# Kernel optimization log

Measured on AMD Instinct MI355X. Metric: run time of the kernel, lower is better.

Reference implementation:

```python
import jax, jax.numpy as jnp
import numpy as np

B, T, E = 2, 2048, 1024
H, D = 16, 64
NH = H * D  # num_hiddens
EPS = 1e-5


def setup_inputs() -> dict:
    key = jax.random.key(0)
    ks = jax.random.split(key, 8)
    s = 1.0 / np.sqrt(E)
    inputs_q = jax.random.normal(ks[0], (B, T, E), dtype=jnp.float32)
    inputs_kv = jax.random.normal(ks[1], (B, T, E), dtype=jnp.float32)
    # torch Linear weights: [out_features, in_features]
    wq = jax.random.uniform(ks[2], (NH, E), jnp.float32, -s, s)
    wk = jax.random.uniform(ks[3], (NH, E), jnp.float32, -s, s)
    wv = jax.random.uniform(ks[4], (NH, E), jnp.float32, -s, s)
    wo = jax.random.uniform(ks[5], (E, NH), jnp.float32, -1.0 / np.sqrt(NH), 1.0 / np.sqrt(NH))
    q_ln_scale = jnp.ones((NH,), jnp.float32)
    q_ln_bias = jnp.zeros((NH,), jnp.float32)
    k_ln_scale = jnp.ones((NH,), jnp.float32)
    k_ln_bias = jnp.zeros((NH,), jnp.float32)
    # causal mask, broadcastable over heads: [B, 1, T, T]
    mask = jnp.broadcast_to(jnp.tril(jnp.ones((T, T), dtype=bool)), (B, 1, T, T))
    return dict(inputs_q=inputs_q, inputs_kv=inputs_kv, mask=mask,
                wq=wq, wk=wk, wv=wv, wo=wo,
                q_ln_scale=q_ln_scale, q_ln_bias=q_ln_bias,
                k_ln_scale=k_ln_scale, k_ln_bias=k_ln_bias)


def _layernorm(x, scale, bias):
    mu = jnp.mean(x, axis=-1, keepdims=True)
    var = jnp.var(x, axis=-1, keepdims=True)
    return (x - mu) * jax.lax.rsqrt(var + EPS) * scale + bias


def reference(inputs_q, inputs_kv, mask, wq, wk, wv, wo,
              q_ln_scale, q_ln_bias, k_ln_scale, k_ln_bias):
    q = jnp.einsum('bte,he->bth', inputs_q, wq)   # [B,T,NH]
    k = jnp.einsum('bte,he->bth', inputs_kv, wk)
    q = _layernorm(q, q_ln_scale, q_ln_bias)
    k = _layernorm(k, k_ln_scale, k_ln_bias)
    v = jnp.einsum('bte,he->bth', inputs_kv, wv)
    q = q.reshape(B, T, H, D)
    k = k.reshape(B, T, H, D)
    v = v.reshape(B, T, H, D)
    attn = jnp.einsum('bthd,bThd->bhtT', q, k) * (1.0 / np.sqrt(D))
    attn = jnp.where(mask, attn, -jnp.inf)
    p = jax.nn.softmax(attn, axis=-1)
    out = jnp.einsum('bhtT,bThd->bthd', p, v).reshape(B, T, NH)
    return jnp.einsum('bth,eh->bte', out, wo)
```

## Files before the change

kernel.cpp:

```cpp
#include <hip/hip_runtime.h>
#include <stdint.h>

#define BB 2
#define TT 2048
#define EE 1024
#define HH 16
#define DD 64
#define NHH 1024
#define BT 4096
#define NT 32

typedef unsigned short u16_t;
typedef __bf16 bf16_t;
typedef bf16_t bf16x8 __attribute__((ext_vector_type(8)));
typedef bf16_t bf16x4 __attribute__((ext_vector_type(4)));
typedef float f32x4 __attribute__((ext_vector_type(4)));

__device__ __forceinline__ u16_t f2bf(float f) {
  union { float f; uint32_t u; } v; v.f = f;
  return (u16_t)((v.u + 0x7fffu + ((v.u >> 16) & 1u)) >> 16);
}

__device__ __forceinline__ uint32_t cvtpk_bf16(float lo, float hi) {
  uint32_t r;
  asm("v_cvt_pk_bf16_f32 %0, %1, %2" : "=v"(r) : "v"(lo), "v"(hi));
  return r;
}

__device__ __forceinline__ void gl_lds16(const u16_t* g, u16_t* l) {
  __builtin_amdgcn_global_load_lds(
      (const __attribute__((address_space(1))) uint32_t*)g,
      (__attribute__((address_space(3))) uint32_t*)l, 16, 0, 0);
}

__global__ __launch_bounds__(256) void cvt_all(const float* __restrict__ inq,
                                               const float* __restrict__ inkv,
                                               const float* __restrict__ wq,
                                               const float* __restrict__ wk,
                                               const float* __restrict__ wv,
                                               const float* __restrict__ wo,
                                               u16_t* __restrict__ Xq,
                                               u16_t* __restrict__ Xkv,
                                               u16_t* __restrict__ Wqkv,
                                               u16_t* __restrict__ Wo) {
  const int NX = BT * NHH / 4;
  const int NW = NHH * EE / 4;
  const int total = 2 * NX + 4 * NW;
  for (int idx = blockIdx.x * 256 + threadIdx.x; idx < total; idx += gridDim.x * 256) {
    const float* src; u16_t* dst; int off;
    if (idx < NX)            { src = inq;  dst = Xq;  off = idx; }
    else if (idx < 2 * NX)   { src = inkv; dst = Xkv; off = idx - NX; }
    else if (idx < 2 * NX + NW)     { src = wq; dst = Wqkv;                       off = idx - 2 * NX; }
    else if (idx < 2 * NX + 2 * NW) { src = wk; dst = Wqkv + (size_t)NHH * EE;    off = idx - (2 * NX + NW); }
    else if (idx < 2 * NX + 3 * NW) { src = wv; dst = Wqkv + (size_t)2 * NHH * EE; off = idx - (2 * NX + 2 * NW); }
    else                            { src = wo; dst = Wo;                          off = idx - (2 * NX + 3 * NW); }
    float4 v = ((const float4*)src)[off];
    ushort4 o;
    o.x = f2bf(v.x); o.y = f2bf(v.y); o.z = f2bf(v.z); o.w = f2bf(v.w);
    ((ushort4*)dst)[off] = o;
  }
}

__global__ __launch_bounds__(256, 3) void gemm_qkv(const u16_t* __restrict__ Xq,
                                                   const u16_t* __restrict__ Xkv,
                                                   const u16_t* __restrict__ Wqkv,
                                                   u16_t* __restrict__ Qpre,
                                                   u16_t* __restrict__ Kpre,
                                                   u16_t* __restrict__ Vt) {
  __shared__ __align__(16) u16_t As[128 * 64];
  __shared__ __align__(16) u16_t Bs[128 * 64];
  const int tid = threadIdx.x;
  const int lane = tid & 63;
  const int w = tid >> 6;
  const int wm = w >> 1, wn = w & 1;
  const int nt = blockIdx.x, mt = blockIdx.y;
  const int l15 = lane & 15, l4 = lane >> 4;
  const int band = nt >> 3;
  const u16_t* A = (band == 0) ? Xq : Xkv;
  const int ncol0 = (nt & 7) * 128;

  f32x4 acc[4][4] = {};
  for (int ks = 0; ks < 16; ++ks) {
    const int k0 = ks << 6;
#pragma unroll
    for (int i = 0; i < 4; ++i) {
      int ci = i * 256 + w * 64 + lane;
      int row = ci >> 3, c8 = ci & 7;
      int c8s = c8 ^ (row & 7);
      gl_lds16(A + (size_t)(mt * 128 + row) * EE + k0 + c8s * 8,
               &As[(i * 256 + w * 64) * 8]);
      gl_lds16(Wqkv + (size_t)(nt * 128 + row) * EE + k0 + c8s * 8,
               &Bs[(i * 256 + w * 64) * 8]);
    }
    __syncthreads();
#pragma unroll
    for (int kt = 0; kt < 2; ++kt) {
      bf16x8 af[4], bfr[4];
#pragma unroll
      for (int m = 0; m < 4; ++m) {
        int r = wm * 64 + m * 16 + l15;
        af[m] = *(const bf16x8*)&As[r * 64 + ((kt * 4 + l4) ^ (r & 7)) * 8];
      }
#pragma unroll
      for (int n = 0; n < 4; ++n) {
        int r = wn * 64 + n * 16 + l15;
        bfr[n] = *(const bf16x8*)&Bs[r * 64 + ((kt * 4 + l4) ^ (r & 7)) * 8];
      }
#pragma unroll
      for (int m = 0; m < 4; ++m)
#pragma unroll
        for (int n = 0; n < 4; ++n)
          acc[m][n] = __builtin_amdgcn_mfma_f32_16x16x32_bf16(af[m], bfr[n], acc[m][n], 0, 0, 0);
    }
    __syncthreads();
  }
  if (band < 2) {
    u16_t* C = (band == 0) ? Qpre : Kpre;
#pragma unroll
    for (int m = 0; m < 4; ++m)
#pragma unroll
      for (int n = 0; n < 4; ++n)
#pragma unroll
        for (int r = 0; r < 4; ++r) {
          int row = mt * 128 + wm * 64 + m * 16 + l4 * 4 + r;
          int col = ncol0 + wn * 64 + n * 16 + l15;
          C[(size_t)row * NHH + col] = f2bf(acc[m][n][r]);
        }
  } else {
#pragma unroll
    for (int m = 0; m < 4; ++m)
#pragma unroll
      for (int n = 0; n < 4; ++n) {
        int rt = mt * 128 + wm * 64 + m * 16 + l4 * 4;
        int col = ncol0 + wn * 64 + n * 16 + l15;
        int bq = rt >> 11, t0 = rt & (TT - 1);
        int hh = col >> 6, dd = col & 63;
        ushort4 o;
        o.x = f2bf(acc[m][n][0]);
        o.y = f2bf(acc[m][n][1]);
        o.z = f2bf(acc[m][n][2]);
        o.w = f2bf(acc[m][n][3]);
        *(ushort4*)&Vt[((size_t)(bq * HH + hh) * 64 + dd) * TT + t0] = o;
      }
  }
}

__global__ __launch_bounds__(256, 3) void gemm_out(const u16_t* __restrict__ A,
                                                   const u16_t* __restrict__ W,
                                                   float* __restrict__ C) {
  __shared__ __align__(16) u16_t As[64 * 64];
  __shared__ __align__(16) u16_t Bs[128 * 64];
  const int tid = threadIdx.x;
  const int lane = tid & 63;
  const int w = tid >> 6;
  const int wm = w >> 1, wn = w & 1;
  const int nt = blockIdx.x, mt = blockIdx.y;
  const int l15 = lane & 15, l4 = lane >> 4;

  f32x4 acc[2][4] = {};
  for (int ks = 0; ks < 16; ++ks) {
    const int k0 = ks << 6;
#pragma unroll
    for (int i = 0; i < 6; ++i) {
      int ci = i * 256 + w * 64 + lane;
      if (i < 2) {
        int row = ci >> 3, c8s = (ci & 7) ^ ((ci >> 3) & 7);
        gl_lds16(A + (size_t)(mt * 64 + row) * NHH + k0 + c8s * 8,
                 &As[(i * 256 + w * 64) * 8]);
      } else {
        int cj = ci - 512;
        int row = cj >> 3, c8s = (cj & 7) ^ ((cj >> 3) & 7);
        gl_lds16(W + (size_t)(nt * 128 + row) * NHH + k0 + c8s * 8,
                 &Bs[(i * 256 + w * 64 - 512) * 8]);
      }
    }
    __syncthreads();
#pragma unroll
    for (int kt = 0; kt < 2; ++kt) {
      bf16x8 af[2], bfr[4];
#pragma unroll
      for (int m = 0; m < 2; ++m) {
        int r = wm * 32 + m * 16 + l15;
        af[m] = *(const bf16x8*)&As[r * 64 + ((kt * 4 + l4) ^ (r & 7)) * 8];
      }
#pragma unroll
      for (int n = 0; n < 4; ++n) {
        int r = wn * 64 + n * 16 + l15;
        bfr[n] = *(const bf16x8*)&Bs[r * 64 + ((kt * 4 + l4) ^ (r & 7)) * 8];
      }
#pragma unroll
      for (int m = 0; m < 2; ++m)
#pragma unroll
        for (int n = 0; n < 4; ++n)
          acc[m][n] = __builtin_amdgcn_mfma_f32_16x16x32_bf16(af[m], bfr[n], acc[m][n], 0, 0, 0);
    }
    __syncthreads();
  }
#pragma unroll
  for (int m = 0; m < 2; ++m)
#pragma unroll
    for (int n = 0; n < 4; ++n)
#pragma unroll
      for (int r = 0; r < 4; ++r) {
        int row = mt * 64 + wm * 32 + m * 16 + l4 * 4 + r;
        int col = nt * 128 + wn * 64 + n * 16 + l15;
        C[(size_t)row * NHH + col] = acc[m][n][r];
      }
}

__global__ __launch_bounds__(256) void ln_both(const u16_t* __restrict__ Qpre,
                                               const u16_t* __restrict__ Kpre,
                                               const float* __restrict__ qs,
                                               const float* __restrict__ qb,
                                               const float* __restrict__ ks,
                                               const float* __restrict__ kb,
                                               u16_t* __restrict__ Qln,
                                               u16_t* __restrict__ Kln) {
  int which = blockIdx.y;
  const u16_t* X = which ? Kpre : Qpre;
  const float* scale = which ? ks : qs;
  const float* bias = which ? kb : qb;
  u16_t* Y = which ? Kln : Qln;
  int row = blockIdx.x;
  int tid = threadIdx.x;
  ushort4 v4 = ((const ushort4*)(X + (size_t)row * NHH))[tid];
  float x[4];
  {
    union { uint32_t u; float f; } c;
    c.u = (uint32_t)v4.x << 16; x[0] = c.f;
    c.u = (uint32_t)v4.y << 16; x[1] = c.f;
    c.u = (uint32_t)v4.z << 16; x[2] = c.f;
    c.u = (uint32_t)v4.w << 16; x[3] = c.f;
  }
  float s = x[0] + x[1] + x[2] + x[3];
  float sq = x[0] * x[0] + x[1] * x[1] + x[2] * x[2] + x[3] * x[3];
#pragma unroll
  for (int m = 1; m < 64; m <<= 1) {
    s += __shfl_xor(s, m);
    sq += __shfl_xor(sq, m);
  }
  __shared__ float ss[4], ssq[4];
  int w = tid >> 6;
  if ((tid & 63) == 0) { ss[w] = s; ssq[w] = sq; }
  __syncthreads();
  s = ss[0] + ss[1] + ss[2] + ss[3];
  sq = ssq[0] + ssq[1] + ssq[2] + ssq[3];
  float mean = s * (1.0f / 1024.0f);
  float var = sq * (1.0f / 1024.0f) - mean * mean;
  float rstd = rsqrtf(var + 1e-5f);
  float4 sc = ((const float4*)scale)[tid];
  float4 bi = ((const float4*)bias)[tid];
  ushort4 o;
  o.x = f2bf((x[0] - mean) * rstd * sc.x + bi.x);
  o.y = f2bf((x[1] - mean) * rstd * sc.y + bi.y);
  o.z = f2bf((x[2] - mean) * rstd * sc.z + bi.z);
  o.w = f2bf((x[3] - mean) * rstd * sc.w + bi.w);
  ((ushort4*)Y)[(size_t)row * 256 + tid] = o;
}

__global__ __launch_bounds__(512, 6) void attn_fwd(const u16_t* __restrict__ Q,
                                                   const u16_t* __restrict__ K,
                                                   const u16_t* __restrict__ Vt,
                                                   u16_t* __restrict__ O) {
  __shared__ __align__(16) u16_t Ks[2][64 * 64];
  __shared__ __align__(16) u16_t Vs[2][64 * 64];
  const int bh = blockIdx.x;
  const int qt = NT - 1 - (int)blockIdx.y;
  const int b = bh >> 4, h = bh & 15;
  const int tid = threadIdx.x, lane = tid & 63, w = tid >> 6;
  const int l15 = lane & 15, l4 = lane >> 4;
  const int qsub = w & 3, par = w >> 2;
  const float SCALE = 0.125f * 1.44269504f;

  const int q0 = qt * 64 + qsub * 16;
  const int myq = q0 + l15;

  bf16x8 qf[2];
#pragma unroll
  for (int kt = 0; kt < 2; ++kt) {
    bf16x8 t = *(const bf16x8*)&Q[(size_t)(b * TT + myq) * NHH + h * 64 + kt * 32 + l4 * 8];
    union { bf16x8 v; uint32_t u[4]; } tt;
    tt.v = t;
#pragma unroll
    for (int d2 = 0; d2 < 4; ++d2) {
      union { uint32_t u; float f; } lo, hi;
      lo.u = tt.u[d2] << 16;
      hi.u = tt.u[d2] & 0xffff0000u;
      tt.u[d2] = cvtpk_bf16(lo.f * SCALE, hi.f * SCALE);
    }
    qf[kt] = tt.v;
  }

  const int ci = tid;
  const int rowk = ci >> 3;
  const int c8k = (ci & 7) ^ (rowk & 7);
  const int c8v = (ci & 7) ^ ((rowk >> 1) & 7);
  const u16_t* kp = K + (size_t)(b * TT + rowk) * NHH + h * 64 + c8k * 8;
  const u16_t* vp = Vt + ((size_t)bh * 64 + rowk) * TT + c8v * 8;
  u16_t* kdst0 = &Ks[0][ci * 8];
  u16_t* kdst1 = &Ks[1][ci * 8];
  u16_t* vdst0 = &Vs[0][ci * 8];
  u16_t* vdst1 = &Vs[1][ci * 8];
  const u16_t* myK = Ks[par];
  const u16_t* myV = Vs[par];

  f32x4 accO[4] = {};
  float lrow = 0.f;

  const int ntile = qt + 1;
  const int nph = (ntile + 1) >> 1;

  for (int ph = 0; ph < nph; ++ph) {
    const int t1ok = (2 * ph + 1) < ntile;
    gl_lds16(kp, kdst0);
    gl_lds16(vp, vdst0);
    if (t1ok) {
      gl_lds16(kp + 64 * NHH, kdst1);
      gl_lds16(vp + 64, vdst1);
    }
    kp += 128 * NHH;
    vp += 128;
    __syncthreads();

    const int t = 2 * ph + par;
    if (t < ntile) {
      const int kb = t * 64;
      const bool masked = (t == qt);
      const int nact = masked ? (qsub + 1) : 4;
      const int ktlim = masked ? ((qsub >> 1) + 1) : 2;

      f32x4 s[4];
      __builtin_amdgcn_s_setprio(1);
#pragma unroll
      for (int n = 0; n < 4; ++n) {
        if (n < nact) {
          s[n] = (f32x4){0.f, 0.f, 0.f, 0.f};
#pragma unroll
          for (int kt = 0; kt < 2; ++kt) {
            int r = n * 16 + l15;
            bf16x8 kf = *(const bf16x8*)&myK[r * 64 + ((kt * 4 + l4) ^ (r & 7)) * 8];
            s[n] = __builtin_amdgcn_mfma_f32_16x16x32_bf16(kf, qf[kt], s[n], 0, 0, 0);
          }
        }
      }
      __builtin_amdgcn_s_setprio(0);
      if (masked) {
#pragma unroll
        for (int n = 0; n < 4; ++n)
          if (n < nact)
#pragma unroll
            for (int r = 0; r < 4; ++r)
              if (kb + n * 16 + l4 * 4 + r > myq) s[n][r] = -3e38f;
      }
      float tsum = 0.f;
#pragma unroll
      for (int n = 0; n < 4; ++n)
        if (n < nact)
#pragma unroll
          for (int r = 0; r < 4; ++r) {
            float p = exp2f(s[n][r]);
            s[n][r] = p;
            tsum += p;
          }
      tsum += __shfl_xor(tsum, 16);
      tsum += __shfl_xor(tsum, 32);
      lrow += tsum;
#pragma unroll
      for (int n = 0; n < 4; ++n)
        if (n >= nact && n < 2 * ktlim) s[n] = (f32x4){0.f, 0.f, 0.f, 0.f};

      __builtin_amdgcn_s_setprio(1);
#pragma unroll
      for (int kt = 0; kt < 2; ++kt) {
        if (kt < ktlim) {
          union { uint32_t u[4]; bf16x8 v; } pa;
          pa.u[0] = cvtpk_bf16(s[2 * kt][0], s[2 * kt][1]);
          pa.u[1] = cvtpk_bf16(s[2 * kt][2], s[2 * kt][3]);
          pa.u[2] = cvtpk_bf16(s[2 * kt + 1][0], s[2 * kt + 1][1]);
          pa.u[3] = cvtpk_bf16(s[2 * kt + 1][2], s[2 * kt + 1][3]);
#pragma unroll
          for (int dn = 0; dn < 4; ++dn) {
            int drow = dn * 16 + l15;
            int vm = l15 & 14;
            int pg0 = (kt * 8 + l4) ^ vm;
            int pg1 = (kt * 8 + 4 + l4) ^ vm;
            union { bf16x4 hh[2]; bf16x8 v; } vf;
            vf.hh[0] = *(const bf16x4*)&myV[drow * 64 + pg0 * 4];
            vf.hh[1] = *(const bf16x4*)&myV[drow * 64 + pg1 * 4];
            accO[dn] = __builtin_amdgcn_mfma_f32_16x16x32_bf16(pa.v, vf.v, accO[dn], 0, 0, 0);
          }
        }
      }
      __builtin_amdgcn_s_setprio(0);
    }
    __syncthreads();
  }

  float* xch = (float*)&Ks[0][0];
  if (par == 1) {
    float* dst = xch + (qsub * 64 + lane) * 20;
#pragma unroll
    for (int dn = 0; dn < 4; ++dn) *(f32x4*)(dst + dn * 4) = accO[dn];
    if (l4 == 0) xch[5120 + qsub * 16 + l15] = lrow;
  } else {
    if (l4 == 0) xch[5184 + qsub * 16 + l15] = lrow;
  }
  __syncthreads();
  if (par == 0) {
    const float* src = xch + (qsub * 64 + lane) * 20;
    f32x4 acc1[4];
#pragma unroll
    for (int dn = 0; dn < 4; ++dn) acc1[dn] = *(const f32x4*)(src + dn * 4);
#pragma unroll
    for (int r = 0; r < 4; ++r) {
      int q = l4 * 4 + r;
      float l0 = xch[5184 + qsub * 16 + q];
      float l1 = xch[5120 + qsub * 16 + q];
      float rinv = 1.0f / (l0 + l1);
      int row = b * TT + q0 + q;
#pragma unroll
      for (int dn = 0; dn < 4; ++dn) {
        float o = (accO[dn][r] + acc1[dn][r]) * rinv;
        O[(size_t)row * NHH + h * 64 + dn * 16 + l15] = f2bf(o);
      }
    }
  }
}

extern "C" void kernel_launch(void* const* d_in, const int* in_sizes, int n_in,
                              void* d_out, int out_size, void* d_ws, size_t ws_size,
                              hipStream_t stream) {
  const float* inq = (const float*)d_in[0];
  const float* inkv = (const float*)d_in[1];
  const float* wq = (const float*)d_in[3];
  const float* wk = (const float*)d_in[4];
  const float* wv = (const float*)d_in[5];
  const float* wo = (const float*)d_in[6];
  const float* qs = (const float*)d_in[7];
  const float* qb = (const float*)d_in[8];
  const float* kls = (const float*)d_in[9];
  const float* klb = (const float*)d_in[10];
  float* out = (float*)d_out;

  uint8_t* ws = (uint8_t*)d_ws;
  const size_t SZ_X = (size_t)BT * NHH * 2;
  const size_t SZ_W = (size_t)NHH * EE * 2;
  u16_t* Xq   = (u16_t*)(ws);
  u16_t* Xkv  = (u16_t*)(ws + SZ_X);
  u16_t* Wqkv = (u16_t*)(ws + 2 * SZ_X);
  u16_t* Wo   = (u16_t*)(ws + 2 * SZ_X + 3 * SZ_W);
  u16_t* Qpre = (u16_t*)(ws + 2 * SZ_X + 4 * SZ_W);
  u16_t* Kpre = (u16_t*)(ws + 3 * SZ_X + 4 * SZ_W);
  u16_t* Qln  = (u16_t*)(ws + 4 * SZ_X + 4 * SZ_W);
  u16_t* Kln  = (u16_t*)(ws + 5 * SZ_X + 4 * SZ_W);
  u16_t* Vt   = (u16_t*)(ws + 6 * SZ_X + 4 * SZ_W);
  u16_t* AOut = (u16_t*)(ws + 7 * SZ_X + 4 * SZ_W);

  cvt_all<<<3072, 256, 0, stream>>>(inq, inkv, wq, wk, wv, wo, Xq, Xkv, Wqkv, Wo);

  gemm_qkv<<<dim3(24, 32), 256, 0, stream>>>(Xq, Xkv, Wqkv, Qpre, Kpre, Vt);

  ln_both<<<dim3(BT, 2), 256, 0, stream>>>(Qpre, Kpre, qs, qb, kls, klb, Qln, Kln);

  attn_fwd<<<dim3(BB * HH, NT), 512, 0, stream>>>(Qln, Kln, Vt, AOut);

  gemm_out<<<dim3(8, 64), 256, 0, stream>>>(AOut, Wo, out);
}
```

Before: 231.6 us.

## Widen attention KV tiles to 128 per wave group and coalesce V-transpose stores

The attention kernel now loads 256 keys per phase (two 128-key halves, one per wave parity) instead of 128. This halves the number of barrier/load phases and doubles the MFMA work per sync. Causal masking now uses a per-subtile relative offset. Occupancy is lowered from 6 to 4 blocks per CU because of the larger LDS footprint. Separately, the QKV GEMM's V output is transposed through shared memory so each thread writes contiguous 16-byte chunks, replacing scattered 8-byte stores.

```diff
diff --git a/kernel.cpp b/kernel.cpp
--- a/kernel.cpp
+++ b/kernel.cpp
@@ -67,8 +67,9 @@
                                                    u16_t* __restrict__ Qpre,
                                                    u16_t* __restrict__ Kpre,
                                                    u16_t* __restrict__ Vt) {
-  __shared__ __align__(16) u16_t As[128 * 64];
-  __shared__ __align__(16) u16_t Bs[128 * 64];
+  __shared__ __align__(16) u16_t smem[128 * 136];
+  u16_t* As = smem;
+  u16_t* Bs = smem + 8192;
   const int tid = threadIdx.x;
   const int lane = tid & 63;
   const int w = tid >> 6;
@@ -131,17 +132,23 @@
     for (int m = 0; m < 4; ++m)
 #pragma unroll
       for (int n = 0; n < 4; ++n) {
-        int rt = mt * 128 + wm * 64 + m * 16 + l4 * 4;
-        int col = ncol0 + wn * 64 + n * 16 + l15;
-        int bq = rt >> 11, t0 = rt & (TT - 1);
-        int hh = col >> 6, dd = col & 63;
-        ushort4 o;
-        o.x = f2bf(acc[m][n][0]);
-        o.y = f2bf(acc[m][n][1]);
-        o.z = f2bf(acc[m][n][2]);
-        o.w = f2bf(acc[m][n][3]);
-        *(ushort4*)&Vt[((size_t)(bq * HH + hh) * 64 + dd) * TT + t0] = o;
-      }
+        int col = wn * 64 + n * 16 + l15;
+        int row0 = wm * 64 + m * 16 + l4 * 4;
+#pragma unroll
+        for (int r = 0; r < 4; ++r)
+          smem[col * 136 + row0 + r] = f2bf(acc[m][n][r]);
+      }
+    __syncthreads();
+    int col = tid >> 1, half = tid & 1;
+    int colg = ncol0 + col;
+    int hh = colg >> 6, dd = colg & 63;
+    int bq = (mt * 128) >> 11;
+    int t0 = (mt * 128) & (TT - 1);
+    u16_t* dst = &Vt[((size_t)(bq * HH + hh) * 64 + dd) * TT + t0 + half * 64];
+    const u16_t* srcp = &smem[col * 136 + half * 64];
+#pragma unroll
+    for (int j = 0; j < 8; ++j)
+      *(uint4*)&dst[j * 8] = *(const uint4*)&srcp[j * 8];
   }
 }
 
@@ -258,12 +265,12 @@
   ((ushort4*)Y)[(size_t)row * 256 + tid] = o;
 }
 
-__global__ __launch_bounds__(512, 6) void attn_fwd(const u16_t* __restrict__ Q,
+__global__ __launch_bounds__(512, 4) void attn_fwd(const u16_t* __restrict__ Q,
                                                    const u16_t* __restrict__ K,
                                                    const u16_t* __restrict__ Vt,
                                                    u16_t* __restrict__ O) {
-  __shared__ __align__(16) u16_t Ks[2][64 * 64];
-  __shared__ __align__(16) u16_t Vs[2][64 * 64];
+  __shared__ __align__(16) u16_t Ks[2][128 * 64];
+  __shared__ __align__(16) u16_t Vs[2][64 * 128];
   const int bh = blockIdx.x;
   const int qt = NT - 1 - (int)blockIdx.y;
   const int b = bh >> 4, h = bh & 15;
@@ -291,48 +298,43 @@
     qf[kt] = tt.v;
   }
 
-  const int ci = tid;
-  const int rowk = ci >> 3;
-  const int c8k = (ci & 7) ^ (rowk & 7);
-  const int c8v = (ci & 7) ^ ((rowk >> 1) & 7);
-  const u16_t* kp = K + (size_t)(b * TT + rowk) * NHH + h * 64 + c8k * 8;
-  const u16_t* vp = Vt + ((size_t)bh * 64 + rowk) * TT + c8v * 8;
-  u16_t* kdst0 = &Ks[0][ci * 8];
-  u16_t* kdst1 = &Ks[1][ci * 8];
-  u16_t* vdst0 = &Vs[0][ci * 8];
-  u16_t* vdst1 = &Vs[1][ci * 8];
+  const u16_t* kbase = K + ((size_t)b * TT) * NHH + h * 64;
+  const u16_t* vbase = Vt + (size_t)bh * 64 * TT;
   const u16_t* myK = Ks[par];
   const u16_t* myV = Vs[par];
 
   f32x4 accO[4] = {};
   float lrow = 0.f;
 
-  const int ntile = qt + 1;
-  const int nph = (ntile + 1) >> 1;
+  const int nph = (qt + 4) >> 2;
 
   for (int ph = 0; ph < nph; ++ph) {
-    const int t1ok = (2 * ph + 1) < ntile;
-    gl_lds16(kp, kdst0);
-    gl_lds16(vp, vdst0);
-    if (t1ok) {
-      gl_lds16(kp + 64 * NHH, kdst1);
-      gl_lds16(vp + 64, vdst1);
-    }
-    kp += 128 * NHH;
-    vp += 128;
-    __syncthreads();
-
-    const int t = 2 * ph + par;
-    if (t < ntile) {
-      const int kb = t * 64;
-      const bool masked = (t == qt);
-      const int nact = masked ? (qsub + 1) : 4;
-      const int ktlim = masked ? ((qsub >> 1) + 1) : 2;
-
-      f32x4 s[4];
+    const int kb0 = ph << 8;
+#pragma unroll
+    for (int ii = 0; ii < 2; ++ii) {
+      int ci = tid + ii * 512;
+      int rowk = ci >> 3, c8s = (ci & 7) ^ (rowk & 7);
+      const u16_t* ksrc = kbase + (size_t)(kb0 + rowk) * NHH + c8s * 8;
+      gl_lds16(ksrc, &Ks[0][ci * 8]);
+      gl_lds16(ksrc + (size_t)128 * NHH, &Ks[1][ci * 8]);
+      int rowv = ci >> 4, c16s = (ci & 15) ^ ((rowv >> 1) & 7);
+      const u16_t* vsrc = vbase + (size_t)rowv * TT + kb0 + c16s * 8;
+      gl_lds16(vsrc, &Vs[0][ci * 8]);
+      gl_lds16(vsrc + 128, &Vs[1][ci * 8]);
+    }
+    __syncthreads();
+
+    const int kbt = kb0 + par * 128;
+    const int rel = q0 + 15 - kbt;
+    if (rel >= 0) {
+      const int nact = min(8, (rel >> 4) + 1);
+      const int ktlim = min(4, (rel >> 5) + 1);
+      const bool domask = (kbt + 127 > q0);
+
+      f32x4 s[8];
       __builtin_amdgcn_s_setprio(1);
 #pragma unroll
-      for (int n = 0; n < 4; ++n) {
+      for (int n = 0; n < 8; ++n) {
         if (n < nact) {
           s[n] = (f32x4){0.f, 0.f, 0.f, 0.f};
 #pragma unroll
@@ -344,17 +346,17 @@
         }
       }
       __builtin_amdgcn_s_setprio(0);
-      if (masked) {
-#pragma unroll
-        for (int n = 0; n < 4; ++n)
+      if (domask) {
+#pragma unroll
+        for (int n = 0; n < 8; ++n)
           if (n < nact)
 #pragma unroll
             for (int r = 0; r < 4; ++r)
-              if (kb + n * 16 + l4 * 4 + r > myq) s[n][r] = -3e38f;
+              if (kbt + n * 16 + l4 * 4 + r > myq) s[n][r] = -3e38f;
       }
       float tsum = 0.f;
 #pragma unroll
-      for (int n = 0; n < 4; ++n)
+      for (int n = 0; n < 8; ++n)
         if (n < nact)
 #pragma unroll
           for (int r = 0; r < 4; ++r) {
@@ -366,12 +368,12 @@
       tsum += __shfl_xor(tsum, 32);
       lrow += tsum;
 #pragma unroll
-      for (int n = 0; n < 4; ++n)
+      for (int n = 0; n < 8; ++n)
         if (n >= nact && n < 2 * ktlim) s[n] = (f32x4){0.f, 0.f, 0.f, 0.f};
 
       __builtin_amdgcn_s_setprio(1);
 #pragma unroll
-      for (int kt = 0; kt < 2; ++kt) {
+      for (int kt = 0; kt < 4; ++kt) {
         if (kt < ktlim) {
           union { uint32_t u[4]; bf16x8 v; } pa;
           pa.u[0] = cvtpk_bf16(s[2 * kt][0], s[2 * kt][1]);
@@ -385,8 +387,8 @@
             int pg0 = (kt * 8 + l4) ^ vm;
             int pg1 = (kt * 8 + 4 + l4) ^ vm;
             union { bf16x4 hh[2]; bf16x8 v; } vf;
-            vf.hh[0] = *(const bf16x4*)&myV[drow * 64 + pg0 * 4];
-            vf.hh[1] = *(const bf16x4*)&myV[drow * 64 + pg1 * 4];
+            vf.hh[0] = *(const bf16x4*)&myV[drow * 128 + pg0 * 4];
+            vf.hh[1] = *(const bf16x4*)&myV[drow * 128 + pg1 * 4];
             accO[dn] = __builtin_amdgcn_mfma_f32_16x16x32_bf16(pa.v, vf.v, accO[dn], 0, 0, 0);
           }
         }
```

New measurement: 227.8 us. Within noise of the previous version (-1.7%).
